# Optimization experiments

Measured on AMD Instinct MI355X. Metric: run time of the kernel, lower is better.

Reference implementation:

```python
import jax, jax.numpy as jnp
import numpy as np

T, D, E, I, TOP_K = 4096, 2048, 8, 4096, 2

def setup_inputs() -> dict:
    key = jax.random.key(0)
    k1, k2, k3, k4, k5 = jax.random.split(key, 5)
    s = 0.02
    return {
        "hidden_states": jax.random.normal(k1, (T, D), jnp.float32),
        "wr": jax.random.normal(k2, (E, D), jnp.float32) * s,
        "w1": jax.random.normal(k3, (E, I, D), jnp.float32) * s,
        "v1": jax.random.normal(k4, (E, I, D), jnp.float32) * s,
        "w2": jax.random.normal(k5, (E, D, I), jnp.float32) * s,
        "index": 0,
    }

def reference(hidden_states, wr, w1, v1, w2, index):
    # index selects the layer; n_layers == 1 here so weights are already that layer's.
    x = hidden_states.reshape(-1, D)  # [T, D]
    # Router logits + softmax top-k with renormalization (fused_moe semantics)
    logits = x @ wr.T                                  # [T, E]
    probs = jax.nn.softmax(logits, axis=-1)
    topw, topi = jax.lax.top_k(probs, TOP_K)           # [T, K]
    topw = topw / jnp.sum(topw, axis=-1, keepdims=True)
    # Dense per-token gate matrix, zero for non-selected experts
    t_idx = jnp.arange(x.shape[0])[:, None]
    gates = jnp.zeros((x.shape[0], E), x.dtype).at[t_idx, topi].set(topw)  # [T, E]
    # SiLU-GLU experts: (silu(x w1^T) * (x v1^T)) w2^T, combined by gates
    out = jnp.zeros_like(x)
    for e in range(E):  # fixed small expert count
        h = jax.nn.silu(x @ w1[e].T) * (x @ v1[e].T)   # [T, I]
        out = out + gates[:, e:e + 1] * (h @ w2[e].T)  # [T, D]
    return out
```

## Files before the change

kernel.cpp:

```cpp
#include <hip/hip_runtime.h>
#include <hip/hip_bf16.h>
#include <cstdint>


#define T_TOK 4096
#define DHID  2048
#define NEXP  8
#define IDIM  4096
#define NSLOT (T_TOK * 2)

#define BM 128
#define BK 64

typedef __bf16 bf16x8 __attribute__((ext_vector_type(8)));
typedef __bf16 bf16x4 __attribute__((ext_vector_type(4)));
typedef float  f32x4  __attribute__((ext_vector_type(4)));

__device__ __forceinline__ void gload_lds16(const void* g, void* l) {
    __builtin_amdgcn_global_load_lds(
        (const __attribute__((address_space(1))) uint32_t*)g,
        (__attribute__((address_space(3))) uint32_t*)l, 16, 0, 0);
}

__global__ __launch_bounds__(256) void router_kernel(
    const float* __restrict__ x, const float* __restrict__ wr,
    __bf16* __restrict__ xb, int* __restrict__ topi, float* __restrict__ topg,
    int* __restrict__ cnt)
{
    int wave = threadIdx.x >> 6, lane = threadIdx.x & 63;
    int t = blockIdx.x * 4 + wave;
    const float4* xr = (const float4*)(x + (size_t)t * DHID);
    bf16x4* xbo = (bf16x4*)(xb + (size_t)t * DHID);
    float acc[NEXP];
#pragma unroll
    for (int e = 0; e < NEXP; ++e) acc[e] = 0.f;
#pragma unroll
    for (int j = 0; j < DHID / 256; ++j) {
        int d4 = lane + j * 64;
        float4 v = xr[d4];
        bf16x4 bv;
        bv[0] = (__bf16)v.x; bv[1] = (__bf16)v.y;
        bv[2] = (__bf16)v.z; bv[3] = (__bf16)v.w;
        xbo[d4] = bv;
#pragma unroll
        for (int e = 0; e < NEXP; ++e) {
            float4 w = ((const float4*)(wr + e * DHID))[d4];
            acc[e] += v.x * w.x + v.y * w.y + v.z * w.z + v.w * w.w;
        }
    }
#pragma unroll
    for (int e = 0; e < NEXP; ++e) {
#pragma unroll
        for (int s = 32; s > 0; s >>= 1) acc[e] += __shfl_xor(acc[e], s);
    }
    if (lane == 0) {
        int e0 = 0; float l0 = acc[0];
#pragma unroll
        for (int e = 1; e < NEXP; ++e) if (acc[e] > l0) { l0 = acc[e]; e0 = e; }
        int e1 = -1; float l1 = -3.4e38f;
#pragma unroll
        for (int e = 0; e < NEXP; ++e) if (e != e0 && acc[e] > l1) { l1 = acc[e]; e1 = e; }
        float g0 = 1.f / (1.f + __expf(l1 - l0));
        topi[t * 2] = e0; topi[t * 2 + 1] = e1;
        topg[t * 2] = g0; topg[t * 2 + 1] = 1.f - g0;
        atomicAdd(&cnt[e0], 1); atomicAdd(&cnt[e1], 1);
    }
}

__global__ void scan_kernel(const int* __restrict__ cnt, int* __restrict__ basep,
                            int* __restrict__ fill)
{
    if (threadIdx.x == 0 && blockIdx.x == 0) {
        int s = 0;
#pragma unroll
        for (int e = 0; e < NEXP; ++e) { basep[e] = s; s += cnt[e]; fill[e] = 0; }
    }
}

__global__ __launch_bounds__(256) void assign_kernel(
    const int* __restrict__ topi, const float* __restrict__ topg,
    const int* __restrict__ basep, int* __restrict__ fill,
    int* __restrict__ tok_of_slot, float* __restrict__ gate_of_slot,
    int* __restrict__ slot_of)
{
    int t = blockIdx.x * 256 + threadIdx.x;
    if (t >= T_TOK) return;
#pragma unroll
    for (int k = 0; k < 2; ++k) {
        int e = topi[t * 2 + k];
        int slot = basep[e] + atomicAdd(&fill[e], 1);
        tok_of_slot[slot] = t;
        gate_of_slot[slot] = topg[t * 2 + k];
        slot_of[t * 2 + k] = slot;
    }
}

__global__ __launch_bounds__(256) void convert_kernel(
    const float* __restrict__ src, __bf16* __restrict__ dst, size_t n8)
{
    for (size_t i = (size_t)blockIdx.x * 256 + threadIdx.x; i < n8;
         i += (size_t)gridDim.x * 256) {
        const float4* s = (const float4*)(src + i * 8);
        float4 a = s[0], b = s[1];
        bf16x8 o;
        o[0]=(__bf16)a.x; o[1]=(__bf16)a.y; o[2]=(__bf16)a.z; o[3]=(__bf16)a.w;
        o[4]=(__bf16)b.x; o[5]=(__bf16)b.y; o[6]=(__bf16)b.z; o[7]=(__bf16)b.w;
        *(bf16x8*)(dst + i * 8) = o;
    }
}

template <int PASS, int KDIM, bool BF16B>
__global__ __launch_bounds__(256, 2) void moe_gemm(
    const __bf16* __restrict__ Abase,
    const void* __restrict__ WaV, const void* __restrict__ WbV,
    const int* __restrict__ tok_of_slot, const float* __restrict__ gate_of_slot,
    const int* __restrict__ cnt, const int* __restrict__ basep,
    __bf16* __restrict__ Out)
{
    int e  = blockIdx.z;
    int ne = cnt[e];
    int m0 = blockIdx.y * BM;
    if (m0 >= ne) return;
    int n0 = blockIdx.x * (PASS == 1 ? 128 : 256);
    int sbase = basep[e] + m0;

    __shared__ __bf16 As[BM * BK];
    __shared__ __bf16 B1s[BM * BK];
    __shared__ __bf16 B2s[BM * BK];
    __shared__ int   toks[BM];
    __shared__ float gates[BM];

    int tid = threadIdx.x, lane = tid & 63, wave = tid >> 6;
    char* AsB = (char*)&As[0];
    char* B1B = (char*)&B1s[0];
    char* B2B = (char*)&B2s[0];

    if (PASS == 1) {
        if (tid < BM) toks[tid] = (m0 + tid < ne) ? tok_of_slot[sbase + tid] : 0;
    } else {
        if (tid < BM) gates[tid] = gate_of_slot[(m0 + tid < ne) ? (sbase + tid) : sbase];
    }
    __syncthreads();

    const __bf16* a_src[4];
    int coff[4];
#pragma unroll
    for (int r = 0; r < 4; ++r) {
        int chunk = wave * 4 + r;
        int arow  = chunk * 8 + (lane >> 3);
        int csw   = (lane & 7) ^ (arow & 7);
        size_t rowbase;
        if (PASS == 1) {
            rowbase = (size_t)toks[arow] * KDIM;
        } else {
            int srow = (m0 + arow < ne) ? (sbase + arow) : sbase;
            rowbase = (size_t)srow * KDIM;
        }
        a_src[r] = Abase + rowbase + csw * 8;
        coff[r]  = chunk * 1024;
    }

    const __bf16* b1_src[4];
    const __bf16* b2_src[4];
    const float *f1_src = nullptr, *f2_src = nullptr;
    int b_woff[4];
    if constexpr (BF16B) {
        const __bf16* Wae;
        const __bf16* Wbe;
        if (PASS == 1) {
            Wae = (const __bf16*)WaV + (size_t)e * IDIM * DHID;
            Wbe = (const __bf16*)WbV + (size_t)e * IDIM * DHID;
        } else {
            Wae = (const __bf16*)WaV + (size_t)e * DHID * IDIM;
            Wbe = Wae + (size_t)128 * KDIM;
        }
#pragma unroll
        for (int r = 0; r < 4; ++r) {
            int chunk = wave * 4 + r;
            int brow  = chunk * 8 + (lane >> 3);
            int csw   = (lane & 7) ^ (brow & 7);
            b1_src[r] = Wae + (size_t)(n0 + brow) * KDIM + csw * 8;
            b2_src[r] = Wbe + (size_t)(n0 + brow) * KDIM + csw * 8;
        }
    } else {
        const float* Wae;
        const float* Wbe;
        if (PASS == 1) {
            Wae = (const float*)WaV + (size_t)e * IDIM * DHID;
            Wbe = (const float*)WbV + (size_t)e * IDIM * DHID;
        } else {
            Wae = (const float*)WaV + (size_t)e * DHID * IDIM;
            Wbe = Wae + (size_t)128 * KDIM;
        }
        int brow = tid >> 1, bh = tid & 1;
        f1_src = Wae + (size_t)(n0 + brow) * KDIM + bh * 32;
        f2_src = Wbe + (size_t)(n0 + brow) * KDIM + bh * 32;
#pragma unroll
        for (int j = 0; j < 4; ++j)
            b_woff[j] = brow * 128 + ((bh * 64 + j * 16) ^ ((brow & 7) << 4));
    }

    int wr0 = (wave >> 1) * 64, wc0 = (wave & 1) * 64;

    f32x4 acc1[4][4], acc2[4][4];
    f32x4 zf = {0.f, 0.f, 0.f, 0.f};
#pragma unroll
    for (int m = 0; m < 4; ++m)
#pragma unroll
        for (int n = 0; n < 4; ++n) { acc1[m][n] = zf; acc2[m][n] = zf; }

    const int NK = KDIM / BK;
    for (int t = 0; t < NK; ++t) {
        int ko = t * BK;
#pragma unroll
        for (int r = 0; r < 4; ++r) gload_lds16(a_src[r] + ko, AsB + coff[r]);
        if constexpr (BF16B) {
#pragma unroll
            for (int r = 0; r < 4; ++r) gload_lds16(b1_src[r] + ko, B1B + coff[r]);
#pragma unroll
            for (int r = 0; r < 4; ++r) gload_lds16(b2_src[r] + ko, B2B + coff[r]);
        } else {
            {
                float4 q[8];
#pragma unroll
                for (int j = 0; j < 8; ++j) q[j] = *(const float4*)(f1_src + ko + j * 4);
#pragma unroll
                for (int j = 0; j < 4; ++j) {
                    float4 fa = q[2 * j], fb = q[2 * j + 1];
                    bf16x8 bv;
                    bv[0]=(__bf16)fa.x; bv[1]=(__bf16)fa.y; bv[2]=(__bf16)fa.z; bv[3]=(__bf16)fa.w;
                    bv[4]=(__bf16)fb.x; bv[5]=(__bf16)fb.y; bv[6]=(__bf16)fb.z; bv[7]=(__bf16)fb.w;
                    *(bf16x8*)(B1B + b_woff[j]) = bv;
                }
            }
            {
                float4 q[8];
#pragma unroll
                for (int j = 0; j < 8; ++j) q[j] = *(const float4*)(f2_src + ko + j * 4);
#pragma unroll
                for (int j = 0; j < 4; ++j) {
                    float4 fa = q[2 * j], fb = q[2 * j + 1];
                    bf16x8 bv;
                    bv[0]=(__bf16)fa.x; bv[1]=(__bf16)fa.y; bv[2]=(__bf16)fa.z; bv[3]=(__bf16)fa.w;
                    bv[4]=(__bf16)fb.x; bv[5]=(__bf16)fb.y; bv[6]=(__bf16)fb.z; bv[7]=(__bf16)fb.w;
                    *(bf16x8*)(B2B + b_woff[j]) = bv;
                }
            }
        }
        __syncthreads();
#pragma unroll
        for (int ks = 0; ks < 2; ++ks) {
            int kb = ks * 64 + (lane >> 4) * 16;
            bf16x8 af[4], b1f[4], b2f[4];
#pragma unroll
            for (int m = 0; m < 4; ++m) {
                int row = wr0 + m * 16 + (lane & 15);
                af[m] = *(const bf16x8*)(AsB + row * 128 + (kb ^ ((row & 7) << 4)));
            }
#pragma unroll
            for (int n = 0; n < 4; ++n) {
                int row = wc0 + n * 16 + (lane & 15);
                int off = row * 128 + (kb ^ ((row & 7) << 4));
                b1f[n] = *(const bf16x8*)(B1B + off);
                b2f[n] = *(const bf16x8*)(B2B + off);
            }
#pragma unroll
            for (int m = 0; m < 4; ++m)
#pragma unroll
                for (int n = 0; n < 4; ++n) {
                    acc1[m][n] = __builtin_amdgcn_mfma_f32_16x16x32_bf16(af[m], b1f[n], acc1[m][n], 0, 0, 0);
                    acc2[m][n] = __builtin_amdgcn_mfma_f32_16x16x32_bf16(af[m], b2f[n], acc2[m][n], 0, 0, 0);
                }
        }
        __syncthreads();
    }

#pragma unroll
    for (int m = 0; m < 4; ++m) {
        int rbase = wr0 + m * 16 + ((lane >> 4) * 4);
#pragma unroll
        for (int n = 0; n < 4; ++n) {
            int col = wc0 + n * 16 + (lane & 15);
#pragma unroll
            for (int r = 0; r < 4; ++r) {
                int lrow = rbase + r;
                if (m0 + lrow < ne) {
                    if (PASS == 1) {
                        float a = acc1[m][n][r];
                        float b = acc2[m][n][r];
                        float h = (a / (1.f + __expf(-a))) * b;
                        Out[(size_t)(sbase + lrow) * IDIM + n0 + col] = (__bf16)h;
                    } else {
                        float g = gates[lrow];
                        size_t obase = (size_t)(sbase + lrow) * DHID + n0;
                        Out[obase + col]       = (__bf16)(acc1[m][n][r] * g);
                        Out[obase + 128 + col] = (__bf16)(acc2[m][n][r] * g);
                    }
                }
            }
        }
    }
}

__global__ __launch_bounds__(256) void combine_kernel(
    const __bf16* __restrict__ outslot, const int* __restrict__ slot_of,
    float* __restrict__ out)
{
    int idx = blockIdx.x * 256 + threadIdx.x;
    int t = idx >> 8;
    int c = (idx & 255) * 8;
    int s0 = slot_of[t * 2], s1 = slot_of[t * 2 + 1];
    bf16x8 a = *(const bf16x8*)(outslot + (size_t)s0 * DHID + c);
    bf16x8 b = *(const bf16x8*)(outslot + (size_t)s1 * DHID + c);
    float4 o0, o1;
    o0.x = (float)a[0] + (float)b[0];
    o0.y = (float)a[1] + (float)b[1];
    o0.z = (float)a[2] + (float)b[2];
    o0.w = (float)a[3] + (float)b[3];
    o1.x = (float)a[4] + (float)b[4];
    o1.y = (float)a[5] + (float)b[5];
    o1.z = (float)a[6] + (float)b[6];
    o1.w = (float)a[7] + (float)b[7];
    *(float4*)(out + (size_t)t * DHID + c)     = o0;
    *(float4*)(out + (size_t)t * DHID + c + 4) = o1;
}

extern "C" void kernel_launch(void* const* d_in, const int* in_sizes, int n_in,
                              void* d_out, int out_size, void* d_ws, size_t ws_size,
                              hipStream_t stream)
{
    (void)in_sizes; (void)n_in; (void)out_size;
    const float* x  = (const float*)d_in[0];
    const float* wr = (const float*)d_in[1];
    const float* w1 = (const float*)d_in[2];
    const float* v1 = (const float*)d_in[3];
    const float* w2 = (const float*)d_in[4];
    float* out = (float*)d_out;

    char* ws = (char*)d_ws;
    size_t off = 0;
    auto alloc = [&](size_t bytes) -> void* {
        void* p = ws + off;
        off += bytes;
        off = (off + 255) & ~(size_t)255;
        return p;
    };
    __bf16* xb      = (__bf16*)alloc((size_t)T_TOK * DHID * 2);
    __bf16* H       = (__bf16*)alloc((size_t)NSLOT * IDIM * 2);
    __bf16* outslot = (__bf16*)alloc((size_t)NSLOT * DHID * 2);
    int*    topi    = (int*)  alloc((size_t)T_TOK * 2 * 4);
    float*  topg    = (float*)alloc((size_t)T_TOK * 2 * 4);
    int*    tok_of_slot  = (int*)  alloc((size_t)NSLOT * 4);
    float*  gate_of_slot = (float*)alloc((size_t)NSLOT * 4);
    int*    slot_of = (int*)  alloc((size_t)NSLOT * 4);
    int*    cnt     = (int*)  alloc(NEXP * 4);
    int*    basep   = (int*)  alloc(NEXP * 4);
    int*    fill    = (int*)  alloc(NEXP * 4);

    const size_t WELEMS = (size_t)NEXP * IDIM * DHID;
    size_t base_need = off;
    bool bf16path = (ws_size >= base_need + 2 * WELEMS * 2 + (32 << 20));

    hipMemsetAsync(cnt, 0, NEXP * 4, stream);
    router_kernel<<<T_TOK / 4, 256, 0, stream>>>(x, wr, xb, topi, topg, cnt);
    scan_kernel<<<1, 64, 0, stream>>>(cnt, basep, fill);
    assign_kernel<<<T_TOK / 256, 256, 0, stream>>>(topi, topg, basep, fill,
                                                   tok_of_slot, gate_of_slot, slot_of);
    if (bf16path) {
        __bf16* wb1 = (__bf16*)alloc(WELEMS * 2);
        __bf16* wv1 = (__bf16*)alloc(WELEMS * 2);
        __bf16* wb2 = wb1;
        convert_kernel<<<2048, 256, 0, stream>>>(w1, wb1, WELEMS / 8);
        convert_kernel<<<2048, 256, 0, stream>>>(v1, wv1, WELEMS / 8);
        moe_gemm<1, DHID, true><<<dim3(IDIM / 128, T_TOK / BM, NEXP), 256, 0, stream>>>(
            xb, wb1, wv1, tok_of_slot, gate_of_slot, cnt, basep, H);
        convert_kernel<<<2048, 256, 0, stream>>>(w2, wb2, WELEMS / 8);
        moe_gemm<2, IDIM, true><<<dim3(DHID / 256, T_TOK / BM, NEXP), 256, 0, stream>>>(
            H, wb2, nullptr, tok_of_slot, gate_of_slot, cnt, basep, outslot);
    } else {
        moe_gemm<1, DHID, false><<<dim3(IDIM / 128, T_TOK / BM, NEXP), 256, 0, stream>>>(
            xb, w1, v1, tok_of_slot, gate_of_slot, cnt, basep, H);
        moe_gemm<2, IDIM, false><<<dim3(DHID / 256, T_TOK / BM, NEXP), 256, 0, stream>>>(
            H, w2, nullptr, tok_of_slot, gate_of_slot, cnt, basep, outslot);
    }
    combine_kernel<<<(T_TOK * DHID / 8) / 256, 256, 0, stream>>>(outslot, slot_of, out);
}
```

Before: 905.6 us.

## Convert expert weights to bf16 in chunks through a small staging buffer

Removes the fallback path where the GEMM kernels read fp32 weights and converted them to bf16 inside every tile. Weights are now always pre-converted, two experts at a time for the first GEMM and four for the second, into a fixed workspace buffer, followed by a bf16 GEMM launch for that expert group. This avoids re-converting fp32 weights for every M-tile and needs much less workspace than converting all experts at once. The cost is extra conversion kernels, serialized per-chunk launches with less parallelism per launch, and a doubled M grid that leaves many blocks exiting early.

```diff
diff --git a/kernel.cpp b/kernel.cpp
--- a/kernel.cpp
+++ b/kernel.cpp
@@ -95,34 +95,46 @@
     }
 }
 
-__global__ __launch_bounds__(256) void convert_kernel(
-    const float* __restrict__ src, __bf16* __restrict__ dst, size_t n8)
+__global__ __launch_bounds__(256) void convert2_kernel(
+    const float* __restrict__ s1, __bf16* __restrict__ d1,
+    const float* __restrict__ s2, __bf16* __restrict__ d2, size_t n8)
 {
     for (size_t i = (size_t)blockIdx.x * 256 + threadIdx.x; i < n8;
          i += (size_t)gridDim.x * 256) {
-        const float4* s = (const float4*)(src + i * 8);
-        float4 a = s[0], b = s[1];
-        bf16x8 o;
-        o[0]=(__bf16)a.x; o[1]=(__bf16)a.y; o[2]=(__bf16)a.z; o[3]=(__bf16)a.w;
-        o[4]=(__bf16)b.x; o[5]=(__bf16)b.y; o[6]=(__bf16)b.z; o[7]=(__bf16)b.w;
-        *(bf16x8*)(dst + i * 8) = o;
-    }
-}
-
-template <int PASS, int KDIM, bool BF16B>
+        {
+            const float4* s = (const float4*)(s1 + i * 8);
+            float4 a = s[0], b = s[1];
+            bf16x8 o;
+            o[0]=(__bf16)a.x; o[1]=(__bf16)a.y; o[2]=(__bf16)a.z; o[3]=(__bf16)a.w;
+            o[4]=(__bf16)b.x; o[5]=(__bf16)b.y; o[6]=(__bf16)b.z; o[7]=(__bf16)b.w;
+            *(bf16x8*)(d1 + i * 8) = o;
+        }
+        if (s2) {
+            const float4* s = (const float4*)(s2 + i * 8);
+            float4 a = s[0], b = s[1];
+            bf16x8 o;
+            o[0]=(__bf16)a.x; o[1]=(__bf16)a.y; o[2]=(__bf16)a.z; o[3]=(__bf16)a.w;
+            o[4]=(__bf16)b.x; o[5]=(__bf16)b.y; o[6]=(__bf16)b.z; o[7]=(__bf16)b.w;
+            *(bf16x8*)(d2 + i * 8) = o;
+        }
+    }
+}
+
+template <int PASS, int KDIM>
 __global__ __launch_bounds__(256, 2) void moe_gemm(
     const __bf16* __restrict__ Abase,
-    const void* __restrict__ WaV, const void* __restrict__ WbV,
+    const __bf16* __restrict__ Wa, const __bf16* __restrict__ Wb,
     const int* __restrict__ tok_of_slot, const float* __restrict__ gate_of_slot,
     const int* __restrict__ cnt, const int* __restrict__ basep,
-    __bf16* __restrict__ Out)
-{
-    int e  = blockIdx.z;
-    int ne = cnt[e];
+    __bf16* __restrict__ Out, int e0)
+{
+    int ez = blockIdx.z;
+    int eg = e0 + ez;
+    int ne = cnt[eg];
     int m0 = blockIdx.y * BM;
     if (m0 >= ne) return;
     int n0 = blockIdx.x * (PASS == 1 ? 128 : 256);
-    int sbase = basep[e] + m0;
+    int sbase = basep[eg] + m0;
 
     __shared__ __bf16 As[BM * BK];
     __shared__ __bf16 B1s[BM * BK];
@@ -162,16 +174,14 @@
 
     const __bf16* b1_src[4];
     const __bf16* b2_src[4];
-    const float *f1_src = nullptr, *f2_src = nullptr;
-    int b_woff[4];
-    if constexpr (BF16B) {
+    {
         const __bf16* Wae;
         const __bf16* Wbe;
         if (PASS == 1) {
-            Wae = (const __bf16*)WaV + (size_t)e * IDIM * DHID;
-            Wbe = (const __bf16*)WbV + (size_t)e * IDIM * DHID;
+            Wae = Wa + (size_t)ez * IDIM * DHID;
+            Wbe = Wb + (size_t)ez * IDIM * DHID;
         } else {
-            Wae = (const __bf16*)WaV + (size_t)e * DHID * IDIM;
+            Wae = Wa + (size_t)ez * DHID * IDIM;
             Wbe = Wae + (size_t)128 * KDIM;
         }
 #pragma unroll
@@ -182,22 +192,6 @@
             b1_src[r] = Wae + (size_t)(n0 + brow) * KDIM + csw * 8;
             b2_src[r] = Wbe + (size_t)(n0 + brow) * KDIM + csw * 8;
         }
-    } else {
-        const float* Wae;
-        const float* Wbe;
-        if (PASS == 1) {
-            Wae = (const float*)WaV + (size_t)e * IDIM * DHID;
-            Wbe = (const float*)WbV + (size_t)e * IDIM * DHID;
-        } else {
-            Wae = (const float*)WaV + (size_t)e * DHID * IDIM;
-            Wbe = Wae + (size_t)128 * KDIM;
-        }
-        int brow = tid >> 1, bh = tid & 1;
-        f1_src = Wae + (size_t)(n0 + brow) * KDIM + bh * 32;
-        f2_src = Wbe + (size_t)(n0 + brow) * KDIM + bh * 32;
-#pragma unroll
-        for (int j = 0; j < 4; ++j)
-            b_woff[j] = brow * 128 + ((bh * 64 + j * 16) ^ ((brow & 7) << 4));
     }
 
     int wr0 = (wave >> 1) * 64, wc0 = (wave & 1) * 64;
@@ -214,39 +208,10 @@
         int ko = t * BK;
 #pragma unroll
         for (int r = 0; r < 4; ++r) gload_lds16(a_src[r] + ko, AsB + coff[r]);
-        if constexpr (BF16B) {
-#pragma unroll
-            for (int r = 0; r < 4; ++r) gload_lds16(b1_src[r] + ko, B1B + coff[r]);
-#pragma unroll
-            for (int r = 0; r < 4; ++r) gload_lds16(b2_src[r] + ko, B2B + coff[r]);
-        } else {
-            {
-                float4 q[8];
-#pragma unroll
-                for (int j = 0; j < 8; ++j) q[j] = *(const float4*)(f1_src + ko + j * 4);
-#pragma unroll
-                for (int j = 0; j < 4; ++j) {
-                    float4 fa = q[2 * j], fb = q[2 * j + 1];
-                    bf16x8 bv;
-                    bv[0]=(__bf16)fa.x; bv[1]=(__bf16)fa.y; bv[2]=(__bf16)fa.z; bv[3]=(__bf16)fa.w;
-                    bv[4]=(__bf16)fb.x; bv[5]=(__bf16)fb.y; bv[6]=(__bf16)fb.z; bv[7]=(__bf16)fb.w;
-                    *(bf16x8*)(B1B + b_woff[j]) = bv;
-                }
-            }
-            {
-                float4 q[8];
-#pragma unroll
-                for (int j = 0; j < 8; ++j) q[j] = *(const float4*)(f2_src + ko + j * 4);
-#pragma unroll
-                for (int j = 0; j < 4; ++j) {
-                    float4 fa = q[2 * j], fb = q[2 * j + 1];
-                    bf16x8 bv;
-                    bv[0]=(__bf16)fa.x; bv[1]=(__bf16)fa.y; bv[2]=(__bf16)fa.z; bv[3]=(__bf16)fa.w;
-                    bv[4]=(__bf16)fb.x; bv[5]=(__bf16)fb.y; bv[6]=(__bf16)fb.z; bv[7]=(__bf16)fb.w;
-                    *(bf16x8*)(B2B + b_woff[j]) = bv;
-                }
-            }
-        }
+#pragma unroll
+        for (int r = 0; r < 4; ++r) gload_lds16(b1_src[r] + ko, B1B + coff[r]);
+#pragma unroll
+        for (int r = 0; r < 4; ++r) gload_lds16(b2_src[r] + ko, B2B + coff[r]);
         __syncthreads();
 #pragma unroll
         for (int ks = 0; ks < 2; ++ks) {
@@ -329,7 +294,7 @@
                               void* d_out, int out_size, void* d_ws, size_t ws_size,
                               hipStream_t stream)
 {
-    (void)in_sizes; (void)n_in; (void)out_size;
+    (void)in_sizes; (void)n_in; (void)out_size; (void)ws_size;
     const float* x  = (const float*)d_in[0];
     const float* wr = (const float*)d_in[1];
     const float* w1 = (const float*)d_in[2];
@@ -357,31 +322,31 @@
     int*    basep   = (int*)  alloc(NEXP * 4);
     int*    fill    = (int*)  alloc(NEXP * 4);
 
-    const size_t WELEMS = (size_t)NEXP * IDIM * DHID;
-    size_t base_need = off;
-    bool bf16path = (ws_size >= base_need + 2 * WELEMS * 2 + (32 << 20));
+    const size_t EW = (size_t)IDIM * DHID;
+    __bf16* chunkbuf = (__bf16*)alloc(4 * EW * 2);
+    __bf16* pb1 = chunkbuf;
+    __bf16* pb2 = chunkbuf + 2 * EW;
+    __bf16* db  = chunkbuf;
 
     hipMemsetAsync(cnt, 0, NEXP * 4, stream);
     router_kernel<<<T_TOK / 4, 256, 0, stream>>>(x, wr, xb, topi, topg, cnt);
     scan_kernel<<<1, 64, 0, stream>>>(cnt, basep, fill);
     assign_kernel<<<T_TOK / 256, 256, 0, stream>>>(topi, topg, basep, fill,
                                                    tok_of_slot, gate_of_slot, slot_of);
-    if (bf16path) {
-        __bf16* wb1 = (__bf16*)alloc(WELEMS * 2);
-        __bf16* wv1 = (__bf16*)alloc(WELEMS * 2);
-        __bf16* wb2 = wb1;
-        convert_kernel<<<2048, 256, 0, stream>>>(w1, wb1, WELEMS / 8);
-        convert_kernel<<<2048, 256, 0, stream>>>(v1, wv1, WELEMS / 8);
-        moe_gemm<1, DHID, true><<<dim3(IDIM / 128, T_TOK / BM, NEXP), 256, 0, stream>>>(
-            xb, wb1, wv1, tok_of_slot, gate_of_slot, cnt, basep, H);
-        convert_kernel<<<2048, 256, 0, stream>>>(w2, wb2, WELEMS / 8);
-        moe_gemm<2, IDIM, true><<<dim3(DHID / 256, T_TOK / BM, NEXP), 256, 0, stream>>>(
-            H, wb2, nullptr, tok_of_slot, gate_of_slot, cnt, basep, outslot);
-    } else {
-        moe_gemm<1, DHID, false><<<dim3(IDIM / 128, T_TOK / BM, NEXP), 256, 0, stream>>>(
-            xb, w1, v1, tok_of_slot, gate_of_slot, cnt, basep, H);
-        moe_gemm<2, IDIM, false><<<dim3(DHID / 256, T_TOK / BM, NEXP), 256, 0, stream>>>(
-            H, w2, nullptr, tok_of_slot, gate_of_slot, cnt, basep, outslot);
+
+    for (int c = 0; c < 4; ++c) {
+        int e0 = c * 2;
+        convert2_kernel<<<2048, 256, 0, stream>>>(
+            w1 + (size_t)e0 * EW, pb1, v1 + (size_t)e0 * EW, pb2, (2 * EW) / 8);
+        moe_gemm<1, DHID><<<dim3(IDIM / 128, NSLOT / BM, 2), 256, 0, stream>>>(
+            xb, pb1, pb2, tok_of_slot, gate_of_slot, cnt, basep, H, e0);
+    }
+    for (int c = 0; c < 2; ++c) {
+        int e0 = c * 4;
+        convert2_kernel<<<2048, 256, 0, stream>>>(
+            w2 + (size_t)e0 * EW, db, nullptr, nullptr, (4 * EW) / 8);
+        moe_gemm<2, IDIM><<<dim3(DHID / 256, NSLOT / BM, 4), 256, 0, stream>>>(
+            H, db, nullptr, tok_of_slot, gate_of_slot, cnt, basep, outslot, e0);
     }
     combine_kernel<<<(T_TOK * DHID / 8) / 256, 256, 0, stream>>>(outslot, slot_of, out);
 }
```

Result: slower. 978.3 us (+8.0%).
